# Kernel tuning notes

Hardware: AMD Instinct MI355X
Metric: run time of the kernel (lower is better)

The kernel has to match this reference:

```python
import jax, jax.numpy as jnp
import numpy as np

PSIZE = 3
PSTRIDE = 3
N = PSIZE * PSTRIDE   # 9 attention tokens
P = PSIZE ** 2        # 9 pixels per token


def setup_inputs() -> dict:
    key = jax.random.key(0)
    k1, k2, k3, k4, k5 = jax.random.split(key, 5)
    B, H, W, C = 8192, 9, 9, 256
    hidden = C // 2
    x = jax.random.normal(k1, (B, H, W, C), dtype=jnp.float32)
    W_fc = jax.random.normal(k2, (hidden, C), dtype=jnp.float32) * (C ** -0.5)
    b_fc = jax.random.normal(k3, (hidden,), dtype=jnp.float32) * 0.01
    block_idx = jax.random.randint(k4, (B,), 0, 1024, dtype=jnp.int32)
    match_vec = jax.random.randint(k5, (1024, 1), 0, 2, dtype=jnp.int32)
    return {"x": x, "W_fc": W_fc, "b_fc": b_fc, "block_idx": block_idx, "match_vec": match_vec}


def reference(x, W_fc, b_fc, block_idx, match_vec):
    B, H, Wd, C = x.shape
    hidden = W_fc.shape[0]
    scale = (hidden * P) ** -0.5

    # [B, pstride, psize, pstride, psize, C] -> patch-major [B, ps, ps, p, p, C]
    xv = x.reshape(B, PSTRIDE, PSIZE, PSTRIDE, PSIZE, C).transpose(0, 1, 3, 2, 4, 5)
    x_fc = xv.reshape(B, N, P, C)

    # linear projection C -> hidden, then flatten pixels: q [B, N, P*hidden]
    q = (jnp.einsum('bnpc,hc->bnph', x_fc, W_fc) + b_fc).reshape(B, N, P * hidden)

    attn = jnp.einsum('bnd,bmd->bnm', q, q) * scale  # [B, N, N]

    # additive mask: -100 on diagonal, zeroed out entirely for matched samples
    base = jnp.where(jnp.eye(N, dtype=bool), jnp.float32(-100.0), jnp.float32(0.0))
    cur_match = match_vec[block_idx].squeeze(-1)  # [B]
    mask = jnp.where(cur_match[:, None, None] == 1, jnp.float32(0.0), base[None])

    attn = jax.nn.softmax(attn + mask, axis=-1)

    v = xv.reshape(B, N, P * C)
    out = attn @ v  # [B, N, P*C]

    out = out.reshape(B, PSTRIDE, PSTRIDE, PSIZE, PSIZE, C)
    out = out.transpose(0, 1, 3, 2, 4, 5).reshape(B, H, Wd, C)
    return out
```

## Files before the change

### kernel.cpp

```cpp
#include <hip/hip_runtime.h>

typedef short short8 __attribute__((ext_vector_type(8)));
typedef float floatx16 __attribute__((ext_vector_type(16)));
typedef float floatx4 __attribute__((ext_vector_type(4)));
typedef unsigned int uint4v __attribute__((ext_vector_type(4)));

#define ROWS 81
#define CDIM 256
#define XOFF 0
#define QOFF 41472
#define SOFF 62208
#define AOFF 63232
#define SMEM_TOTAL 63616

__device__ __forceinline__ unsigned short f2bf(float f) {
    union { float f; unsigned int u; } v; v.f = f;
    return (unsigned short)((v.u + 0x7FFFu + ((v.u >> 16) & 1u)) >> 16);
}

__global__ void wconv_kernel(const float* __restrict__ W,
                             unsigned short* __restrict__ Wb, int n) {
    int i = blockIdx.x * 256 + threadIdx.x;
    if (i < n) Wb[i] = f2bf(W[i]);
}

__global__ __launch_bounds__(256, 2)
void attn_kernel(const float* __restrict__ x,
                 const unsigned short* __restrict__ Wb,
                 const float* __restrict__ b_fc,
                 const int* __restrict__ block_idx,
                 const int* __restrict__ match_vec,
                 float* __restrict__ out)
{
    __shared__ __align__(16) char smem[SMEM_TOTAL];
    const int b    = blockIdx.x;
    const int t    = threadIdx.x;
    const int lane = t & 63;
    const int wave = t >> 6;
    const int lrow = lane & 31;
    const int khalf = lane >> 5;

    int cur_match = 0;
    if (t < 9) cur_match = match_vec[block_idx[b]];

    short8 bfrag[16];
    {
        const unsigned short* wr = Wb + (wave * 32 + lrow) * CDIM;
#pragma unroll
        for (int ks = 0; ks < 16; ++ks)
            bfrag[ks] = *(const short8*)(wr + ks * 16 + khalf * 8);
    }
    const float bias = b_fc[wave * 32 + lrow];

    {
        const float* xb = x + (long)b * (ROWS * CDIM);
        for (int k = t; k < ROWS * 32; k += 256) {
            int gr = k >> 5;
            int c0 = (k & 31) * 8;
            float4 a0 = *(const float4*)(xb + gr * CDIM + c0);
            float4 a1 = *(const float4*)(xb + gr * CDIM + c0 + 4);
            int hh = gr / 9, ww = gr % 9;
            int r = ((hh / 3) * 3 + (ww / 3)) * 9 + ((hh % 3) * 3 + (ww % 3));
            short8 v;
            v[0] = (short)f2bf(a0.x); v[1] = (short)f2bf(a0.y);
            v[2] = (short)f2bf(a0.z); v[3] = (short)f2bf(a0.w);
            v[4] = (short)f2bf(a1.x); v[5] = (short)f2bf(a1.y);
            v[6] = (short)f2bf(a1.z); v[7] = (short)f2bf(a1.w);
            int off = r * 512 + ((c0 * 2) ^ ((r & 15) << 4));
            *(short8*)(smem + off) = v;
        }
    }
    __syncthreads();

    floatx16 acc0, acc1, acc2;
#pragma unroll
    for (int i = 0; i < 16; ++i) { acc0[i] = 0.f; acc1[i] = 0.f; acc2[i] = 0.f; }
    const int sw = (lrow & 15) << 4;
#pragma unroll
    for (int ks = 0; ks < 16; ++ks) {
        int cb = (ks * 32 + khalf * 16) ^ sw;
        short8 a0 = *(const short8*)(smem + (lrow      ) * 512 + cb);
        short8 a1 = *(const short8*)(smem + (lrow + 32 ) * 512 + cb);
        short8 a2 = *(const short8*)(smem + (lrow + 64 ) * 512 + cb);
        acc0 = __builtin_amdgcn_mfma_f32_32x32x16_bf16(a0, bfrag[ks], acc0, 0, 0, 0);
        acc1 = __builtin_amdgcn_mfma_f32_32x32x16_bf16(a1, bfrag[ks], acc1, 0, 0, 0);
        acc2 = __builtin_amdgcn_mfma_f32_32x32x16_bf16(a2, bfrag[ks], acc2, 0, 0, 0);
    }

    {
        int hcol2 = (wave * 32 + lrow) * 2;
#pragma unroll
        for (int reg = 0; reg < 16; ++reg) {
            int rb = (reg & 3) + 8 * (reg >> 2) + 4 * khalf;
            int r0 = rb, r1 = rb + 32, r2 = rb + 64;
            *(unsigned short*)(smem + QOFF + r0 * 256 + (hcol2 ^ ((r0 & 15) << 4))) = f2bf(acc0[reg] + bias);
            *(unsigned short*)(smem + QOFF + r1 * 256 + (hcol2 ^ ((r1 & 15) << 4))) = f2bf(acc1[reg] + bias);
            if (r2 < ROWS)
                *(unsigned short*)(smem + QOFF + r2 * 256 + (hcol2 ^ ((r2 & 15) << 4))) = f2bf(acc2[reg] + bias);
        }
    }
    __syncthreads();

    if (wave == 0) {
        floatx4 sacc;
#pragma unroll
        for (int i = 0; i < 4; ++i) sacc[i] = 0.f;
        int n  = lane & 15;
        int nc = (n < 9) ? n : 8;
        int kg = lane >> 4;
#pragma unroll
        for (int ks = 0; ks < 36; ++ks) {
            int k  = ks * 32 + kg * 8;
            int p  = k >> 7;
            int h0 = (k & 127) * 2;
            int row = nc * 9 + p;
            short8 f = *(const short8*)(smem + QOFF + row * 256 + (h0 ^ ((row & 15) << 4)));
            sacc = __builtin_amdgcn_mfma_f32_16x16x32_bf16(f, f, sacc, 0, 0, 0);
        }
        float* sc = (float*)(smem + SOFF);
#pragma unroll
        for (int reg = 0; reg < 4; ++reg)
            sc[(kg * 4 + reg) * 16 + n] = sacc[reg];
    }
    __syncthreads();

    if (t < 9) {
        const float scale = 0.029462782549439483f;
        float* sc = (float*)(smem + SOFF);
        float* at = (float*)(smem + AOFF);
        float s[9];
        float mx = -1e30f;
#pragma unroll
        for (int m = 0; m < 9; ++m) {
            float v = sc[t * 16 + m] * scale;
            if (m == t && cur_match != 1) v -= 100.f;
            s[m] = v;
            mx = fmaxf(mx, v);
        }
        float sum = 0.f;
#pragma unroll
        for (int m = 0; m < 9; ++m) { s[m] = __expf(s[m] - mx); sum += s[m]; }
        float inv = 1.f / sum;
#pragma unroll
        for (int m = 0; m < 9; ++m) at[t * 9 + m] = s[m] * inv;
    }
    __syncthreads();

    {
        const float* at = (const float*)(smem + AOFF);
        float* ob = out + (long)b * (ROWS * CDIM);
        for (int k = t; k < ROWS * 32; k += 256) {
            int r  = k >> 5;
            int c0 = (k & 31) * 8;
            int n = r / 9, p = r % 9;
            float o[8];
#pragma unroll
            for (int i = 0; i < 8; ++i) o[i] = 0.f;
#pragma unroll
            for (int m = 0; m < 9; ++m) {
                float a = at[n * 9 + m];
                int row = m * 9 + p;
                uint4v u = *(const uint4v*)(smem + row * 512 + ((c0 * 2) ^ ((row & 15) << 4)));
                o[0] += a * __uint_as_float(u.x << 16);
                o[1] += a * __uint_as_float(u.x & 0xffff0000u);
                o[2] += a * __uint_as_float(u.y << 16);
                o[3] += a * __uint_as_float(u.y & 0xffff0000u);
                o[4] += a * __uint_as_float(u.z << 16);
                o[5] += a * __uint_as_float(u.z & 0xffff0000u);
                o[6] += a * __uint_as_float(u.w << 16);
                o[7] += a * __uint_as_float(u.w & 0xffff0000u);
            }
            int hh = (n / 3) * 3 + (p / 3);
            int ww = (n % 3) * 3 + (p % 3);
            int gr = hh * 9 + ww;
            *(float4*)(ob + gr * CDIM + c0)     = make_float4(o[0], o[1], o[2], o[3]);
            *(float4*)(ob + gr * CDIM + c0 + 4) = make_float4(o[4], o[5], o[6], o[7]);
        }
    }
}

extern "C" void kernel_launch(void* const* d_in, const int* in_sizes, int n_in,
                              void* d_out, int out_size, void* d_ws, size_t ws_size,
                              hipStream_t stream) {
    const float* x    = (const float*)d_in[0];
    const float* W    = (const float*)d_in[1];
    const float* bfc  = (const float*)d_in[2];
    const int*   bidx = (const int*)d_in[3];
    const int*   mvec = (const int*)d_in[4];
    float* outp = (float*)d_out;
    unsigned short* Wb = (unsigned short*)d_ws;

    int nW = in_sizes[1];
    wconv_kernel<<<(nW + 255) / 256, 256, 0, stream>>>(W, Wb, nW);

    int B = in_sizes[0] / (ROWS * CDIM);
    attn_kernel<<<B, 256, 0, stream>>>(x, Wb, bfc, bidx, mvec, outp);
}
```

Measured before the change: 390.5 us.

## Retile projection to 16x16 MFMA across 8 waves and use MFMA for attn@V

Doubles the block to 512 threads so each of 8 waves computes 16 hidden columns with 16x16x32 MFMAs over six row tiles. The score MFMA chain is split into four independent accumulators to shorten the dependency chain. The attention-times-V step moves from scalar FMAs to a 32x32x16 bf16 MFMA, with the softmax weights stored in LDS as padded bf16. In exchange, attention weights lose precision, most MFMA columns are wasted on padding, the V operand is gathered with per-element short LDS loads, and stores become fragmented 16-byte writes from only 9 of 32 lanes.

```diff
diff --git a/kernel.cpp b/kernel.cpp
--- a/kernel.cpp
+++ b/kernel.cpp
@@ -7,11 +7,10 @@
 
 #define ROWS 81
 #define CDIM 256
-#define XOFF 0
 #define QOFF 41472
 #define SOFF 62208
-#define AOFF 63232
-#define SMEM_TOTAL 63616
+#define ABOFF 63232
+#define SMEM_TOTAL 63744
 
 __device__ __forceinline__ unsigned short f2bf(float f) {
     union { float f; unsigned int u; } v; v.f = f;
@@ -24,7 +23,7 @@
     if (i < n) Wb[i] = f2bf(W[i]);
 }
 
-__global__ __launch_bounds__(256, 2)
+__global__ __launch_bounds__(512, 4)
 void attn_kernel(const float* __restrict__ x,
                  const unsigned short* __restrict__ Wb,
                  const float* __restrict__ b_fc,
@@ -33,28 +32,30 @@
                  float* __restrict__ out)
 {
     __shared__ __align__(16) char smem[SMEM_TOTAL];
-    const int b    = blockIdx.x;
-    const int t    = threadIdx.x;
-    const int lane = t & 63;
-    const int wave = t >> 6;
-    const int lrow = lane & 31;
+    const int b     = blockIdx.x;
+    const int t     = threadIdx.x;
+    const int lane  = t & 63;
+    const int wave  = t >> 6;
+    const int l15   = lane & 15;
+    const int kg    = lane >> 4;
+    const int l31   = lane & 31;
     const int khalf = lane >> 5;
 
     int cur_match = 0;
     if (t < 9) cur_match = match_vec[block_idx[b]];
 
-    short8 bfrag[16];
-    {
-        const unsigned short* wr = Wb + (wave * 32 + lrow) * CDIM;
-#pragma unroll
-        for (int ks = 0; ks < 16; ++ks)
-            bfrag[ks] = *(const short8*)(wr + ks * 16 + khalf * 8);
-    }
-    const float bias = b_fc[wave * 32 + lrow];
+    short8 wfrag[8];
+    {
+        const unsigned short* wr = Wb + (wave * 16 + l15) * CDIM + kg * 8;
+#pragma unroll
+        for (int ks = 0; ks < 8; ++ks)
+            wfrag[ks] = *(const short8*)(wr + ks * 32);
+    }
+    const float bias = b_fc[wave * 16 + l15];
 
     {
         const float* xb = x + (long)b * (ROWS * CDIM);
-        for (int k = t; k < ROWS * 32; k += 256) {
+        for (int k = t; k < ROWS * 32; k += 512) {
             int gr = k >> 5;
             int c0 = (k & 31) * 8;
             float4 a0 = *(const float4*)(xb + gr * CDIM + c0);
@@ -72,62 +73,67 @@
     }
     __syncthreads();
 
-    floatx16 acc0, acc1, acc2;
-#pragma unroll
-    for (int i = 0; i < 16; ++i) { acc0[i] = 0.f; acc1[i] = 0.f; acc2[i] = 0.f; }
-    const int sw = (lrow & 15) << 4;
-#pragma unroll
-    for (int ks = 0; ks < 16; ++ks) {
-        int cb = (ks * 32 + khalf * 16) ^ sw;
-        short8 a0 = *(const short8*)(smem + (lrow      ) * 512 + cb);
-        short8 a1 = *(const short8*)(smem + (lrow + 32 ) * 512 + cb);
-        short8 a2 = *(const short8*)(smem + (lrow + 64 ) * 512 + cb);
-        acc0 = __builtin_amdgcn_mfma_f32_32x32x16_bf16(a0, bfrag[ks], acc0, 0, 0, 0);
-        acc1 = __builtin_amdgcn_mfma_f32_32x32x16_bf16(a1, bfrag[ks], acc1, 0, 0, 0);
-        acc2 = __builtin_amdgcn_mfma_f32_32x32x16_bf16(a2, bfrag[ks], acc2, 0, 0, 0);
-    }
-
-    {
-        int hcol2 = (wave * 32 + lrow) * 2;
-#pragma unroll
-        for (int reg = 0; reg < 16; ++reg) {
-            int rb = (reg & 3) + 8 * (reg >> 2) + 4 * khalf;
-            int r0 = rb, r1 = rb + 32, r2 = rb + 64;
-            *(unsigned short*)(smem + QOFF + r0 * 256 + (hcol2 ^ ((r0 & 15) << 4))) = f2bf(acc0[reg] + bias);
-            *(unsigned short*)(smem + QOFF + r1 * 256 + (hcol2 ^ ((r1 & 15) << 4))) = f2bf(acc1[reg] + bias);
-            if (r2 < ROWS)
-                *(unsigned short*)(smem + QOFF + r2 * 256 + (hcol2 ^ ((r2 & 15) << 4))) = f2bf(acc2[reg] + bias);
+    floatx4 acc[6];
+#pragma unroll
+    for (int i = 0; i < 6; ++i)
+#pragma unroll
+        for (int j = 0; j < 4; ++j) acc[i][j] = 0.f;
+    const int swl = l15 << 4;
+#pragma unroll
+    for (int ks = 0; ks < 8; ++ks) {
+        int cb = ks * 64 + kg * 16;
+#pragma unroll
+        for (int tile = 0; tile < 6; ++tile) {
+            int r = tile * 16 + l15;
+            short8 a = *(const short8*)(smem + r * 512 + (cb ^ swl));
+            acc[tile] = __builtin_amdgcn_mfma_f32_16x16x32_bf16(a, wfrag[ks], acc[tile], 0, 0, 0);
+        }
+    }
+
+    {
+        int h2 = (wave * 16 + l15) * 2;
+#pragma unroll
+        for (int tile = 0; tile < 6; ++tile) {
+#pragma unroll
+            for (int reg = 0; reg < 4; ++reg) {
+                int r = tile * 16 + kg * 4 + reg;
+                if (r < ROWS)
+                    *(unsigned short*)(smem + QOFF + r * 256 + (h2 ^ ((r & 15) << 4))) =
+                        f2bf(acc[tile][reg] + bias);
+            }
         }
     }
     __syncthreads();
 
     if (wave == 0) {
-        floatx4 sacc;
-#pragma unroll
-        for (int i = 0; i < 4; ++i) sacc[i] = 0.f;
-        int n  = lane & 15;
-        int nc = (n < 9) ? n : 8;
-        int kg = lane >> 4;
-#pragma unroll
-        for (int ks = 0; ks < 36; ++ks) {
-            int k  = ks * 32 + kg * 8;
-            int p  = k >> 7;
-            int h0 = (k & 127) * 2;
-            int row = nc * 9 + p;
-            short8 f = *(const short8*)(smem + QOFF + row * 256 + (h0 ^ ((row & 15) << 4)));
-            sacc = __builtin_amdgcn_mfma_f32_16x16x32_bf16(f, f, sacc, 0, 0, 0);
+        floatx4 s0, s1, s2, s3;
+#pragma unroll
+        for (int i = 0; i < 4; ++i) { s0[i] = 0.f; s1[i] = 0.f; s2[i] = 0.f; s3[i] = 0.f; }
+        int nc = (l15 < 9) ? l15 : 8;
+#pragma unroll
+        for (int s = 0; s < 9; ++s) {
+#pragma unroll
+            for (int i = 0; i < 4; ++i) {
+                int ks = i * 9 + s;
+                int k  = ks * 32 + kg * 8;
+                int p  = k >> 7;
+                int h0 = (k & 127) * 2;
+                int row = nc * 9 + p;
+                short8 f = *(const short8*)(smem + QOFF + row * 256 + (h0 ^ ((row & 15) << 4)));
+                floatx4 tmp = __builtin_amdgcn_mfma_f32_16x16x32_bf16(f, f, (i==0?s0:i==1?s1:i==2?s2:s3), 0, 0, 0);
+                if (i == 0) s0 = tmp; else if (i == 1) s1 = tmp; else if (i == 2) s2 = tmp; else s3 = tmp;
+            }
         }
         float* sc = (float*)(smem + SOFF);
 #pragma unroll
         for (int reg = 0; reg < 4; ++reg)
-            sc[(kg * 4 + reg) * 16 + n] = sacc[reg];
+            sc[(kg * 4 + reg) * 16 + l15] = s0[reg] + s1[reg] + s2[reg] + s3[reg];
     }
     __syncthreads();
 
     if (t < 9) {
         const float scale = 0.029462782549439483f;
         float* sc = (float*)(smem + SOFF);
-        float* at = (float*)(smem + AOFF);
         float s[9];
         float mx = -1e30f;
 #pragma unroll
@@ -141,40 +147,48 @@
 #pragma unroll
         for (int m = 0; m < 9; ++m) { s[m] = __expf(s[m] - mx); sum += s[m]; }
         float inv = 1.f / sum;
-#pragma unroll
-        for (int m = 0; m < 9; ++m) at[t * 9 + m] = s[m] * inv;
-    }
-    __syncthreads();
-
-    {
-        const float* at = (const float*)(smem + AOFF);
+        unsigned short* ab = (unsigned short*)(smem + ABOFF) + t * 16;
+#pragma unroll
+        for (int m = 0; m < 9; ++m) ab[m] = f2bf(s[m] * inv);
+#pragma unroll
+        for (int m = 9; m < 16; ++m) ab[m] = 0;
+    }
+    __syncthreads();
+
+    {
+        const int n  = l31;
+        const int nm = (n < 9) ? n : 0;
+        short8 bf = *(const short8*)(smem + ABOFF + nm * 32 + khalf * 16);
         float* ob = out + (long)b * (ROWS * CDIM);
-        for (int k = t; k < ROWS * 32; k += 256) {
-            int r  = k >> 5;
-            int c0 = (k & 31) * 8;
-            int n = r / 9, p = r % 9;
-            float o[8];
-#pragma unroll
-            for (int i = 0; i < 8; ++i) o[i] = 0.f;
-#pragma unroll
-            for (int m = 0; m < 9; ++m) {
-                float a = at[n * 9 + m];
+        int hh = 0, ww = 0;
+        if (n < 9) { hh = (n / 3) * 3; ww = (n % 3) * 3; }
+#pragma unroll
+        for (int tt = 0; tt < 9; ++tt) {
+            int tile = wave * 9 + tt;
+            int d = tile * 32 + l31;
+            int p = d >> 8, c = d & 255;
+            short8 af;
+#pragma unroll
+            for (int j = 0; j < 8; ++j) {
+                int m = khalf * 8 + j; if (m > 8) m = 8;
                 int row = m * 9 + p;
-                uint4v u = *(const uint4v*)(smem + row * 512 + ((c0 * 2) ^ ((row & 15) << 4)));
-                o[0] += a * __uint_as_float(u.x << 16);
-                o[1] += a * __uint_as_float(u.x & 0xffff0000u);
-                o[2] += a * __uint_as_float(u.y << 16);
-                o[3] += a * __uint_as_float(u.y & 0xffff0000u);
-                o[4] += a * __uint_as_float(u.z << 16);
-                o[5] += a * __uint_as_float(u.z & 0xffff0000u);
-                o[6] += a * __uint_as_float(u.w << 16);
-                o[7] += a * __uint_as_float(u.w & 0xffff0000u);
-            }
-            int hh = (n / 3) * 3 + (p / 3);
-            int ww = (n % 3) * 3 + (p % 3);
-            int gr = hh * 9 + ww;
-            *(float4*)(ob + gr * CDIM + c0)     = make_float4(o[0], o[1], o[2], o[3]);
-            *(float4*)(ob + gr * CDIM + c0 + 4) = make_float4(o[4], o[5], o[6], o[7]);
+                af[j] = *(const short*)(smem + row * 512 + ((c * 2) ^ ((row & 15) << 4)));
+            }
+            floatx16 dacc;
+#pragma unroll
+            for (int i = 0; i < 16; ++i) dacc[i] = 0.f;
+            dacc = __builtin_amdgcn_mfma_f32_32x32x16_bf16(af, bf, dacc, 0, 0, 0);
+            if (n < 9) {
+#pragma unroll
+                for (int q2 = 0; q2 < 4; ++q2) {
+                    int d0 = tile * 32 + q2 * 8 + khalf * 4;
+                    int p0 = d0 >> 8, c0 = d0 & 255;
+                    int gr = (hh + (p0 / 3)) * 9 + (ww + (p0 % 3));
+                    *(float4*)(ob + gr * CDIM + c0) =
+                        make_float4(dacc[q2 * 4 + 0], dacc[q2 * 4 + 1],
+                                    dacc[q2 * 4 + 2], dacc[q2 * 4 + 3]);
+                }
+            }
         }
     }
 }
@@ -194,5 +208,5 @@
     wconv_kernel<<<(nW + 255) / 256, 256, 0, stream>>>(W, Wb, nW);
 
     int B = in_sizes[0] / (ROWS * CDIM);
-    attn_kernel<<<B, 256, 0, stream>>>(x, Wb, bfc, bidx, mvec, outp);
-}
+    attn_kernel<<<B, 512, 0, stream>>>(x, Wb, bfc, bidx, mvec, outp);
+}
```

New measurement: 371.4 us. 1.05x faster.
